# Kernel optimization log

Measured on AMD Instinct MI355X. Metric: run time of the kernel, lower is better.

Reference implementation:

```python
import jax, jax.numpy as jnp
import numpy as np

S, B, IN, OUT = 2048, 8, 1024, 4096
ALPHA = 0.5  # SmoothQuant migration strength (scaling_factor)
QMAX = 127.0  # symmetric int8


def _ste_round(t):
    # straight-through round (matches pytorch_quantization fake-quant)
    return t + jax.lax.stop_gradient(jnp.round(t) - t)


def _fake_quant(t):
    # per-tensor symmetric int8 fake quantization
    amax = jax.lax.stop_gradient(jnp.max(jnp.abs(t)))
    s = jnp.where(amax > 0, amax / QMAX, jnp.float32(1.0))
    return jnp.clip(_ste_round(t / s), -QMAX, QMAX) * s


def setup_inputs() -> dict:
    key = jax.random.key(0)
    k1, k2, k3 = jax.random.split(key, 3)
    x = jax.random.normal(k1, (S, B, IN), dtype=jnp.float32)
    weight = jax.random.normal(k2, (OUT, IN), dtype=jnp.float32) * 0.02
    bias = jax.random.normal(k3, (OUT,), dtype=jnp.float32) * 0.01
    return {"x": x, "weight": weight, "bias": bias}


def reference(x, weight, bias):
    seq, bs, _ = x.shape
    x2 = x.reshape(-1, IN)  # [S*B, IN]
    # dynamic per-input-channel scales (detached in the original)
    w_scale = jnp.max(jnp.abs(jax.lax.stop_gradient(weight)), axis=0)   # [IN]
    act_scale = jnp.max(jnp.abs(jax.lax.stop_gradient(x2)), axis=0)     # [IN]
    scale = act_scale ** ALPHA / w_scale ** (1.0 - ALPHA)
    scale = jnp.where(scale == 0, jnp.float32(1.0), scale)
    w = _fake_quant(weight * scale)   # [OUT, IN]
    xq = _fake_quant(x2 / scale)      # [S*B, IN]
    out = xq @ w.T + bias[None, :]    # [S*B, OUT]
    return out.reshape(-1, bs, OUT)
```

## Files before the change

kernel.cpp:

```cpp
#include <hip/hip_runtime.h>

#define IN_DIM  1024
#define OUT_DIM 4096
#define M_DIM   16384
#define QMAXF   127.0f

typedef int v4i __attribute__((ext_vector_type(4)));

__global__ void colmax_kernel(const float* __restrict__ in, unsigned* __restrict__ outb,
                              int rows, int cols, int rpb) {
    int j  = blockIdx.x * blockDim.x + threadIdx.x;
    int r0 = blockIdx.y * rpb;
    int r1 = r0 + rpb; if (r1 > rows) r1 = rows;
    float m = 0.f;
    for (int r = r0; r < r1; ++r)
        m = fmaxf(m, fabsf(in[(size_t)r * cols + j]));
    atomicMax(&outb[j], __float_as_uint(m));
}

__global__ void scale_amax_kernel(float* __restrict__ wsf) {
    int j = threadIdx.x;
    float wsc = wsf[j];
    float asc = wsf[1024 + j];
    float s = sqrtf(asc) / sqrtf(wsc);
    if (s == 0.0f) s = 1.0f;
    wsf[2048 + j] = s;
    float aw = wsc * s;
    float ax = asc / s;
    int lane = j & 63, wid = j >> 6;
    #pragma unroll
    for (int off = 32; off; off >>= 1) {
        aw = fmaxf(aw, __shfl_down(aw, off));
        ax = fmaxf(ax, __shfl_down(ax, off));
    }
    __shared__ float rw[16], rx[16];
    if (lane == 0) { rw[wid] = aw; rx[wid] = ax; }
    __syncthreads();
    if (j == 0) {
        float mw = rw[0], mx = rx[0];
        #pragma unroll
        for (int i = 1; i < 16; ++i) { mw = fmaxf(mw, rw[i]); mx = fmaxf(mx, rx[i]); }
        wsf[3072] = mw;
        wsf[3073] = mx;
    }
}

__global__ void quant_kernel(const float4* __restrict__ in, const float* __restrict__ scale,
                             const float* __restrict__ amaxp, unsigned* __restrict__ out8,
                             int n4, int div) {
    float amax = *amaxp;
    float qs = amax > 0.f ? amax / QMAXF : 1.0f;
    int stride = gridDim.x * blockDim.x;
    for (int i = blockIdx.x * blockDim.x + threadIdx.x; i < n4; i += stride) {
        float4 v = in[i];
        int j = (i << 2) & (IN_DIM - 1);
        float s0 = scale[j], s1 = scale[j + 1], s2 = scale[j + 2], s3 = scale[j + 3];
        float t0, t1, t2, t3;
        if (div) { t0 = v.x / s0; t1 = v.y / s1; t2 = v.z / s2; t3 = v.w / s3; }
        else     { t0 = v.x * s0; t1 = v.y * s1; t2 = v.z * s2; t3 = v.w * s3; }
        int q0 = (int)fminf(fmaxf(rintf(t0 / qs), -QMAXF), QMAXF);
        int q1 = (int)fminf(fmaxf(rintf(t1 / qs), -QMAXF), QMAXF);
        int q2 = (int)fminf(fmaxf(rintf(t2 / qs), -QMAXF), QMAXF);
        int q3 = (int)fminf(fmaxf(rintf(t3 / qs), -QMAXF), QMAXF);
        out8[i] = (q0 & 0xff) | ((q1 & 0xff) << 8) | ((q2 & 0xff) << 16) | ((q3 & 0xff) << 24);
    }
}

#define BM 128
#define BN 128
#define BK 128

__device__ __forceinline__ void load_lds16(const void* g, void* l) {
    __builtin_amdgcn_global_load_lds((const __attribute__((address_space(1))) void*)g,
                                     (__attribute__((address_space(3))) void*)l, 16, 0, 0);
}

__global__ __launch_bounds__(256) void gemm_i8_kernel(
    const char* __restrict__ Xq, const char* __restrict__ Wq,
    const float* __restrict__ bias, const float* __restrict__ wsf,
    float* __restrict__ out) {
    __shared__ char As[BM * BK];
    __shared__ char Bs[BN * BK];
    const int K = IN_DIM, N = OUT_DIM;
    int tid  = threadIdx.x;
    int lane = tid & 63, w = tid >> 6;
    int bn0 = blockIdx.x * BN, bm0 = blockIdx.y * BM;
    int wrow = (w >> 1) * 64, wcol = (w & 1) * 64;
    int l15 = lane & 15, l4 = lane >> 4;
    int swz = (lane & 7) << 4;

    v4i acc[4][4];
    #pragma unroll
    for (int i = 0; i < 4; ++i)
        #pragma unroll
        for (int jj = 0; jj < 4; ++jj)
            acc[i][jj] = (v4i){0, 0, 0, 0};

    for (int kt = 0; kt < K / BK; ++kt) {
        int k0 = kt * BK;
        #pragma unroll
        for (int q = 0; q < 4; ++q) {
            int c = q * 256 + w * 64 + lane;
            int row = c >> 3, slot = c & 7;
            int col = (slot * 16) ^ ((row & 7) << 4);
            load_lds16(Xq + (size_t)(bm0 + row) * K + k0 + col, As + q * 4096 + w * 1024);
            load_lds16(Wq + (size_t)(bn0 + row) * K + k0 + col, Bs + q * 4096 + w * 1024);
        }
        __syncthreads();
        #pragma unroll
        for (int kk = 0; kk < 2; ++kk) {
            int coff = ((kk << 6) | (l4 << 4)) ^ swz;
            v4i a[4], b[4];
            #pragma unroll
            for (int am = 0; am < 4; ++am)
                a[am] = *(const v4i*)(As + (wrow + am * 16 + l15) * BK + coff);
            #pragma unroll
            for (int bb = 0; bb < 4; ++bb)
                b[bb] = *(const v4i*)(Bs + (wcol + bb * 16 + l15) * BK + coff);
            #pragma unroll
            for (int am = 0; am < 4; ++am)
                #pragma unroll
                for (int bb = 0; bb < 4; ++bb)
                    acc[am][bb] = __builtin_amdgcn_mfma_i32_16x16x64_i8(a[am], b[bb], acc[am][bb], 0, 0, 0);
        }
        __syncthreads();
    }

    float amw = wsf[3072], amx = wsf[3073];
    float sw = amw > 0.f ? amw / QMAXF : 1.0f;
    float sx = amx > 0.f ? amx / QMAXF : 1.0f;
    float sp = sw * sx;

    #pragma unroll
    for (int am = 0; am < 4; ++am) {
        int row = bm0 + wrow + am * 16 + l4 * 4;
        #pragma unroll
        for (int bb = 0; bb < 4; ++bb) {
            int col = bn0 + wcol + bb * 16 + l15;
            float bv = bias[col];
            #pragma unroll
            for (int r = 0; r < 4; ++r)
                out[(size_t)(row + r) * N + col] = fmaf(sp, (float)acc[am][bb][r], bv);
        }
    }
}

extern "C" void kernel_launch(void* const* d_in, const int* in_sizes, int n_in,
                              void* d_out, int out_size, void* d_ws, size_t ws_size,
                              hipStream_t stream) {
    const float* x      = (const float*)d_in[0];
    const float* weight = (const float*)d_in[1];
    const float* bias   = (const float*)d_in[2];
    float* out = (float*)d_out;

    float*    wsf = (float*)d_ws;
    unsigned* wsu = (unsigned*)d_ws;
    char* X8 = (char*)d_ws + 16384;
    char* W8 = X8 + (size_t)M_DIM * IN_DIM;

    hipMemsetAsync(d_ws, 0, 16384, stream);

    colmax_kernel<<<dim3(IN_DIM / 256, 16),  256, 0, stream>>>(weight, wsu,        OUT_DIM, IN_DIM, 256);
    colmax_kernel<<<dim3(IN_DIM / 256, 128), 256, 0, stream>>>(x,      wsu + 1024, M_DIM,   IN_DIM, 128);

    scale_amax_kernel<<<1, 1024, 0, stream>>>(wsf);

    quant_kernel<<<1024, 256, 0, stream>>>((const float4*)weight, wsf + 2048, wsf + 3072,
                                           (unsigned*)W8, OUT_DIM * IN_DIM / 4, 0);
    quant_kernel<<<2048, 256, 0, stream>>>((const float4*)x, wsf + 2048, wsf + 3073,
                                           (unsigned*)X8, M_DIM * IN_DIM / 4, 1);

    gemm_i8_kernel<<<dim3(OUT_DIM / BN, M_DIM / BM), 256, 0, stream>>>(X8, W8, bias, wsf, out);
}
```

Before: 557.4 us.

## Vectorize column-max, fuse quant kernels, and swizzle GEMM block order

The column-max reduction now reads float4 rows with one block per row chunk, replacing scalar per-column loads. The two quantization launches become one fused kernel that loads the per-channel scale as float4 instead of four scalars. The GEMM remaps its linear block index so that blocks scheduled close together share input tiles, aiming for better L2 reuse. Together these aim to cut memory-bound preprocessing time and launch overhead, at the cost of a branch inside the fused loop.

```diff
diff --git a/kernel.cpp b/kernel.cpp
--- a/kernel.cpp
+++ b/kernel.cpp
@@ -7,15 +7,25 @@
 
 typedef int v4i __attribute__((ext_vector_type(4)));
 
-__global__ void colmax_kernel(const float* __restrict__ in, unsigned* __restrict__ outb,
-                              int rows, int cols, int rpb) {
-    int j  = blockIdx.x * blockDim.x + threadIdx.x;
-    int r0 = blockIdx.y * rpb;
+__global__ void colmax4_kernel(const float4* __restrict__ in, unsigned* __restrict__ outb,
+                               int rows, int rpb) {
+    int t  = threadIdx.x;
+    int r0 = blockIdx.x * rpb;
     int r1 = r0 + rpb; if (r1 > rows) r1 = rows;
-    float m = 0.f;
-    for (int r = r0; r < r1; ++r)
-        m = fmaxf(m, fabsf(in[(size_t)r * cols + j]));
-    atomicMax(&outb[j], __float_as_uint(m));
+    float m0 = 0.f, m1 = 0.f, m2 = 0.f, m3 = 0.f;
+    #pragma unroll 4
+    for (int r = r0; r < r1; ++r) {
+        float4 v = in[(size_t)r * 256 + t];
+        m0 = fmaxf(m0, fabsf(v.x));
+        m1 = fmaxf(m1, fabsf(v.y));
+        m2 = fmaxf(m2, fabsf(v.z));
+        m3 = fmaxf(m3, fabsf(v.w));
+    }
+    unsigned* o = outb + t * 4;
+    atomicMax(o + 0, __float_as_uint(m0));
+    atomicMax(o + 1, __float_as_uint(m1));
+    atomicMax(o + 2, __float_as_uint(m2));
+    atomicMax(o + 3, __float_as_uint(m3));
 }
 
 __global__ void scale_amax_kernel(float* __restrict__ wsf) {
@@ -45,24 +55,36 @@
     }
 }
 
-__global__ void quant_kernel(const float4* __restrict__ in, const float* __restrict__ scale,
-                             const float* __restrict__ amaxp, unsigned* __restrict__ out8,
-                             int n4, int div) {
-    float amax = *amaxp;
-    float qs = amax > 0.f ? amax / QMAXF : 1.0f;
+#define NW4 (OUT_DIM * IN_DIM / 4)
+#define NX4 (M_DIM * IN_DIM / 4)
+
+__device__ __forceinline__ unsigned pack_q4(float t0, float t1, float t2, float t3, float qs) {
+    int q0 = (int)fminf(fmaxf(rintf(t0 / qs), -QMAXF), QMAXF);
+    int q1 = (int)fminf(fmaxf(rintf(t1 / qs), -QMAXF), QMAXF);
+    int q2 = (int)fminf(fmaxf(rintf(t2 / qs), -QMAXF), QMAXF);
+    int q3 = (int)fminf(fmaxf(rintf(t3 / qs), -QMAXF), QMAXF);
+    return (q0 & 0xff) | ((q1 & 0xff) << 8) | ((q2 & 0xff) << 16) | ((q3 & 0xff) << 24);
+}
+
+__global__ void quant_fused_kernel(const float4* __restrict__ w, const float4* __restrict__ x,
+                                   const float* __restrict__ wsf,
+                                   unsigned* __restrict__ w8, unsigned* __restrict__ x8) {
+    const float4* scale4 = (const float4*)(wsf + 2048);
+    float amw = wsf[3072], amx = wsf[3073];
+    float qsw = amw > 0.f ? amw / QMAXF : 1.0f;
+    float qsx = amx > 0.f ? amx / QMAXF : 1.0f;
     int stride = gridDim.x * blockDim.x;
-    for (int i = blockIdx.x * blockDim.x + threadIdx.x; i < n4; i += stride) {
-        float4 v = in[i];
-        int j = (i << 2) & (IN_DIM - 1);
-        float s0 = scale[j], s1 = scale[j + 1], s2 = scale[j + 2], s3 = scale[j + 3];
-        float t0, t1, t2, t3;
-        if (div) { t0 = v.x / s0; t1 = v.y / s1; t2 = v.z / s2; t3 = v.w / s3; }
-        else     { t0 = v.x * s0; t1 = v.y * s1; t2 = v.z * s2; t3 = v.w * s3; }
-        int q0 = (int)fminf(fmaxf(rintf(t0 / qs), -QMAXF), QMAXF);
-        int q1 = (int)fminf(fmaxf(rintf(t1 / qs), -QMAXF), QMAXF);
-        int q2 = (int)fminf(fmaxf(rintf(t2 / qs), -QMAXF), QMAXF);
-        int q3 = (int)fminf(fmaxf(rintf(t3 / qs), -QMAXF), QMAXF);
-        out8[i] = (q0 & 0xff) | ((q1 & 0xff) << 8) | ((q2 & 0xff) << 16) | ((q3 & 0xff) << 24);
+    for (int i = blockIdx.x * blockDim.x + threadIdx.x; i < NW4 + NX4; i += stride) {
+        if (i < NW4) {
+            float4 v = w[i];
+            float4 s = scale4[i & 255];
+            w8[i] = pack_q4(v.x * s.x, v.y * s.y, v.z * s.z, v.w * s.w, qsw);
+        } else {
+            int k = i - NW4;
+            float4 v = x[k];
+            float4 s = scale4[k & 255];
+            x8[k] = pack_q4(v.x / s.x, v.y / s.y, v.z / s.z, v.w / s.w, qsx);
+        }
     }
 }
 
@@ -84,10 +106,14 @@
     const int K = IN_DIM, N = OUT_DIM;
     int tid  = threadIdx.x;
     int lane = tid & 63, w = tid >> 6;
-    int bn0 = blockIdx.x * BN, bm0 = blockIdx.y * BM;
+
+    int lin = blockIdx.y * gridDim.x + blockIdx.x;
+    int swz = (lin & 7) * 512 + (lin >> 3);
+    int bn0 = (swz & 31) * BN, bm0 = (swz >> 5) * BM;
+
     int wrow = (w >> 1) * 64, wcol = (w & 1) * 64;
     int l15 = lane & 15, l4 = lane >> 4;
-    int swz = (lane & 7) << 4;
+    int swzl = (lane & 7) << 4;
 
     v4i acc[4][4];
     #pragma unroll
@@ -109,7 +135,7 @@
         __syncthreads();
         #pragma unroll
         for (int kk = 0; kk < 2; ++kk) {
-            int coff = ((kk << 6) | (l4 << 4)) ^ swz;
+            int coff = ((kk << 6) | (l4 << 4)) ^ swzl;
             v4i a[4], b[4];
             #pragma unroll
             for (int am = 0; am < 4; ++am)
@@ -160,15 +186,13 @@
 
     hipMemsetAsync(d_ws, 0, 16384, stream);
 
-    colmax_kernel<<<dim3(IN_DIM / 256, 16),  256, 0, stream>>>(weight, wsu,        OUT_DIM, IN_DIM, 256);
-    colmax_kernel<<<dim3(IN_DIM / 256, 128), 256, 0, stream>>>(x,      wsu + 1024, M_DIM,   IN_DIM, 128);
+    colmax4_kernel<<<256, 256, 0, stream>>>((const float4*)weight, wsu,        OUT_DIM, 16);
+    colmax4_kernel<<<256, 256, 0, stream>>>((const float4*)x,      wsu + 1024, M_DIM,   64);
 
     scale_amax_kernel<<<1, 1024, 0, stream>>>(wsf);
 
-    quant_kernel<<<1024, 256, 0, stream>>>((const float4*)weight, wsf + 2048, wsf + 3072,
-                                           (unsigned*)W8, OUT_DIM * IN_DIM / 4, 0);
-    quant_kernel<<<2048, 256, 0, stream>>>((const float4*)x, wsf + 2048, wsf + 3073,
-                                           (unsigned*)X8, M_DIM * IN_DIM / 4, 1);
+    quant_fused_kernel<<<2560, 256, 0, stream>>>((const float4*)weight, (const float4*)x,
+                                                 wsf, (unsigned*)W8, (unsigned*)X8);
 
     gemm_i8_kernel<<<dim3(OUT_DIM / BN, M_DIM / BM), 256, 0, stream>>>(X8, W8, bias, wsf, out);
 }
```

Result: faster. 462.1 us (-17.1%).
